# Kernel optimization log

Measured on AMD Instinct MI355X. Metric: run time of the kernel, lower is better.

## Reference

```python
import jax, jax.numpy as jnp
import numpy as np

D_MODEL = 1024
N_HEADS = 16
HEAD_DIM = D_MODEL // N_HEADS
B, S = 2, 2048


def setup_inputs() -> dict:
    key = jax.random.key(0)
    k1, k2, k3, k4, k5 = jax.random.split(key, 5)
    scale = 1.0 / np.sqrt(D_MODEL)
    return {
        "x": jax.random.normal(k1, (B, S, D_MODEL), dtype=jnp.float32),
        "mask": jnp.ones((B, S), dtype=jnp.int32),
        "W_qkv": jax.random.normal(k2, (D_MODEL, 3 * D_MODEL), dtype=jnp.float32) * scale,
        "b_qkv": jnp.zeros((3 * D_MODEL,), dtype=jnp.float32),
        "W_proj": jax.random.normal(k3, (D_MODEL, D_MODEL), dtype=jnp.float32) * scale,
        "b_proj": jnp.zeros((D_MODEL,), dtype=jnp.float32),
    }


def reference(x, mask, W_qkv, b_qkv, W_proj, b_proj):
    b, s, d = x.shape
    qkv = x @ W_qkv + b_qkv                                  # [B,S,3D]
    qkv = qkv.reshape(b, s, 3, N_HEADS, HEAD_DIM)
    qkv = jnp.transpose(qkv, (2, 0, 3, 1, 4))                # [3,B,H,S,Dh]
    q, k, v = qkv[0], qkv[1], qkv[2]
    scores = jnp.einsum("bhqd,bhkd->bhqk", q, k) / np.sqrt(HEAD_DIM)
    if mask is not None:
        m = mask[:, None, None, :]                           # [B,1,1,S]
        scores = jnp.where(m == 0, -jnp.inf, scores)
    attn = jax.nn.softmax(scores, axis=-1)
    out = jnp.einsum("bhqk,bhkd->bhqd", attn, v)             # [B,H,S,Dh]
    out = jnp.transpose(out, (0, 2, 1, 3)).reshape(b, s, d)  # [B,S,D]
    return out @ W_proj + b_proj
```

## Files before the change

kernel.cpp:

```cpp
#include <hip/hip_runtime.h>

typedef unsigned short u16;
typedef unsigned int u32;
typedef __bf16 bf16x8 __attribute__((ext_vector_type(8)));
typedef float f32x4 __attribute__((ext_vector_type(4)));
typedef float f32x16 __attribute__((ext_vector_type(16)));

#define D_MODEL 1024
#define SQ 2048
#define NH 16
#define HD 64
#define QSCALE 0.1803368801111204f

__device__ __forceinline__ u16 f2bf(float f) {
    u32 u = __builtin_bit_cast(u32, f);
    u = (u + 0x7fffu + ((u >> 16) & 1u)) >> 16;
    return (u16)u;
}

__device__ __forceinline__ f32x4 mfma16(bf16x8 a, bf16x8 b, f32x4 c) {
    return __builtin_amdgcn_mfma_f32_16x16x32_bf16(a, b, c, 0, 0, 0);
}
__device__ __forceinline__ f32x16 mfma32(bf16x8 a, bf16x8 b, f32x16 c) {
    return __builtin_amdgcn_mfma_f32_32x32x16_bf16(a, b, c, 0, 0, 0);
}

__device__ __forceinline__ bf16x8 ld16(const void* p) {
    return __builtin_bit_cast(bf16x8, *(const int4*)p);
}

__device__ __forceinline__ void gl_lds16(const u16* g, u16* l) {
    __builtin_amdgcn_global_load_lds((const __attribute__((address_space(1))) unsigned int*)g,
                                     (__attribute__((address_space(3))) unsigned int*)l, 16, 0, 0);
}

__device__ __forceinline__ u32 cvtpk(float a, float b) {
    u32 r;
    asm("v_cvt_pk_bf16_f32 %0, %1, %2" : "=v"(r) : "v"(a), "v"(b));
    return r;
}

__device__ __forceinline__ void swap32(u32& a, u32& b) {
    asm("v_permlane32_swap_b32 %0, %1" : "+v"(a), "+v"(b));
}


__global__ __launch_bounds__(256) void cvt_f32_bf16(const float* __restrict__ in,
                                                    u16* __restrict__ out, int n4) {
    int i = blockIdx.x * blockDim.x + threadIdx.x;
    if (i >= n4) return;
    float4 v = ((const float4*)in)[i];
    ushort4 o;
    o.x = f2bf(v.x); o.y = f2bf(v.y); o.z = f2bf(v.z); o.w = f2bf(v.w);
    ((ushort4*)out)[i] = o;
}

__global__ __launch_bounds__(256) void tconv(const float* __restrict__ in,
                                             u16* __restrict__ out, int K, int N) {
    __shared__ float t[32][33];
    const int n0 = blockIdx.x * 32, k0 = blockIdx.y * 32;
    const int tx = threadIdx.x, ty = threadIdx.y;
#pragma unroll
    for (int i = 0; i < 4; ++i)
        t[ty + 8 * i][tx] = in[(size_t)(k0 + ty + 8 * i) * N + n0 + tx];
    __syncthreads();
#pragma unroll
    for (int i = 0; i < 4; ++i)
        out[(size_t)(n0 + ty + 8 * i) * K + k0 + tx] = f2bf(t[tx][ty + 8 * i]);
}

__global__ __launch_bounds__(256) void vtrans(const u16* __restrict__ Vw, u16* __restrict__ Vtw) {
    __shared__ u16 T[64][72];
    const int bh = blockIdx.y, s0 = blockIdx.x * 64, tid = threadIdx.x;
    const int r = tid >> 3, cb = tid & 7;
#pragma unroll
    for (int i = 0; i < 2; ++i) {
        int rr = r + 32 * i;
        int4 v = *(const int4*)(Vw + ((size_t)bh * SQ + s0 + rr) * HD + cb * 8);
        *(int4*)&T[rr][cb * 8] = v;
    }
    __syncthreads();
#pragma unroll
    for (int i = 0; i < 2; ++i) {
        int d = r + 32 * i, so = cb * 8;
        u16 tmp[8];
#pragma unroll
        for (int j = 0; j < 8; ++j) tmp[j] = T[so + j][d];
        *(int4*)(Vtw + ((size_t)bh * HD + d) * SQ + s0 + so) = *(int4*)tmp;
    }
}


template <int MODE>
__global__ __launch_bounds__(256) void gemm128(const u16* __restrict__ A,
                                               const u16* __restrict__ Bt,
                                               const float* __restrict__ bias,
                                               u16* __restrict__ Qw, u16* __restrict__ Kw,
                                               u16* __restrict__ Vw, float* __restrict__ Out) {
    __shared__ u16 As[128 * 32];
    __shared__ u16 Bs[128 * 32];

    const int tid = threadIdx.x;
    const int l = tid & 63, w = tid >> 6;
    const int l16 = l & 15, lq = l >> 4;
    const int wm = w >> 1, wn = w & 1;
    const int m0 = blockIdx.y * 128, n0 = blockIdx.x * 128;

    f32x4 acc[4][4];
#pragma unroll
    for (int i = 0; i < 4; ++i)
#pragma unroll
        for (int j = 0; j < 4; ++j) acc[i][j] = f32x4{0.f, 0.f, 0.f, 0.f};

    const int srow = 32 * w + (l >> 2);
    const u16* aSrc = A + (size_t)(m0 + srow) * 1024 + (l & 3) * 8;
    const u16* bSrc = Bt + (size_t)(n0 + srow) * 1024 + (l & 3) * 8;
    u16* AsW = As + w * 1024;
    u16* BsW = Bs + w * 1024;

    for (int kt = 0; kt < 32; ++kt) {
        __syncthreads();
        gl_lds16(aSrc + kt * 32, AsW);
        gl_lds16(aSrc + kt * 32 + (size_t)16 * 1024, AsW + 512);
        gl_lds16(bSrc + kt * 32, BsW);
        gl_lds16(bSrc + kt * 32 + (size_t)16 * 1024, BsW + 512);
        __syncthreads();

        bf16x8 af[4], bfr[4];
#pragma unroll
        for (int mi = 0; mi < 4; ++mi)
            af[mi] = ld16((char*)As + (wm * 64 + mi * 16 + l16) * 64 + lq * 16);
#pragma unroll
        for (int ni = 0; ni < 4; ++ni)
            bfr[ni] = ld16((char*)Bs + (wn * 64 + ni * 16 + l16) * 64 + lq * 16);
#pragma unroll
        for (int mi = 0; mi < 4; ++mi)
#pragma unroll
            for (int ni = 0; ni < 4; ++ni)
                acc[mi][ni] = mfma16(af[mi], bfr[ni], acc[mi][ni]);
    }

#pragma unroll
    for (int mi = 0; mi < 4; ++mi) {
#pragma unroll
        for (int ni = 0; ni < 4; ++ni) {
            const int n = n0 + wn * 64 + ni * 16 + l16;
            const float bv = bias[n];
#pragma unroll
            for (int r = 0; r < 4; ++r) {
                const int m = m0 + wm * 64 + mi * 16 + 4 * lq + r;
                float v = acc[mi][ni][r] + bv;
                if (MODE == 0) {
                    const int which = n >> 10;
                    const int h = (n >> 6) & 15;
                    const int d = n & 63;
                    const int b = m >> 11, s = m & 2047;
                    const size_t bh = (size_t)(b * NH + h);
                    if (which == 0)
                        Qw[(bh * SQ + s) * HD + d] = f2bf(v * QSCALE);
                    else if (which == 1)
                        Kw[(bh * SQ + s) * HD + d] = f2bf(v);
                    else
                        Vw[(bh * SQ + s) * HD + d] = f2bf(v);
                } else {
                    Out[(size_t)m * 1024 + n] = v;
                }
            }
        }
    }
}


__global__ __launch_bounds__(256) void gemm_proj(const u16* __restrict__ A,
                                                 const u16* __restrict__ Bt,
                                                 const float* __restrict__ bias,
                                                 float* __restrict__ Out) {
    __shared__ u16 As[128 * 32];
    __shared__ u16 Bs[64 * 32];

    const int tid = threadIdx.x;
    const int l = tid & 63, w = tid >> 6;
    const int l16 = l & 15, lq = l >> 4;
    const int wm = w >> 1, wn = w & 1;
    const int m0 = blockIdx.y * 128, n0 = blockIdx.x * 64;

    f32x4 acc[4][2];
#pragma unroll
    for (int i = 0; i < 4; ++i)
#pragma unroll
        for (int j = 0; j < 2; ++j) acc[i][j] = f32x4{0.f, 0.f, 0.f, 0.f};

    const int srowA = 32 * w + (l >> 2);
    const int srowB = 16 * w + (l >> 2);
    const u16* aSrc = A + (size_t)(m0 + srowA) * 1024 + (l & 3) * 8;
    const u16* bSrc = Bt + (size_t)(n0 + srowB) * 1024 + (l & 3) * 8;
    u16* AsW = As + w * 1024;
    u16* BsW = Bs + w * 512;

    for (int kt = 0; kt < 32; ++kt) {
        __syncthreads();
        gl_lds16(aSrc + kt * 32, AsW);
        gl_lds16(aSrc + kt * 32 + (size_t)16 * 1024, AsW + 512);
        gl_lds16(bSrc + kt * 32, BsW);
        __syncthreads();

        bf16x8 af[4], bfr[2];
#pragma unroll
        for (int mi = 0; mi < 4; ++mi)
            af[mi] = ld16((char*)As + (wm * 64 + mi * 16 + l16) * 64 + lq * 16);
#pragma unroll
        for (int ni = 0; ni < 2; ++ni)
            bfr[ni] = ld16((char*)Bs + (wn * 32 + ni * 16 + l16) * 64 + lq * 16);
#pragma unroll
        for (int mi = 0; mi < 4; ++mi)
#pragma unroll
            for (int ni = 0; ni < 2; ++ni)
                acc[mi][ni] = mfma16(af[mi], bfr[ni], acc[mi][ni]);
    }

#pragma unroll
    for (int mi = 0; mi < 4; ++mi) {
#pragma unroll
        for (int ni = 0; ni < 2; ++ni) {
            const int n = n0 + wn * 32 + ni * 16 + l16;
            const float bv = bias[n];
#pragma unroll
            for (int r = 0; r < 4; ++r) {
                const int m = m0 + wm * 64 + mi * 16 + 4 * lq + r;
                Out[(size_t)m * 1024 + n] = acc[mi][ni][r] + bv;
            }
        }
    }
}


__global__ __launch_bounds__(256, 4) void attn64(const u16* __restrict__ Qw, const u16* __restrict__ Kw,
                                                 const u16* __restrict__ Vtw, const int* __restrict__ mask,
                                                 u16* __restrict__ Ow) {
    __shared__ u16 Ks[2][64 * 64];
    __shared__ u16 Vs[2][64 * 64];
    __shared__ u16 smadd16[SQ];
    __shared__ int allFlag;

    const int tid = threadIdx.x;
    const int l = tid & 63, w = tid >> 6;
    const int q = l & 31, hl = l >> 5;
    const int qh = w & 1, kb = w >> 1;
    const int bh = blockIdx.y, b = bh >> 4, h = bh & 15;
    const int q0 = blockIdx.x * 64;

    if (tid == 0) allFlag = 1;
    __syncthreads();
    {
        const int4* m4 = (const int4*)(mask + (size_t)b * SQ) + tid * 2;
        int4 a0 = m4[0], a1 = m4[1];
        int ok = a0.x && a0.y && a0.z && a0.w && a1.x && a1.y && a1.z && a1.w;
        const u16 NEG = f2bf(-1e30f);
        u16* sp = &smadd16[tid * 8];
        sp[0] = a0.x ? (u16)0 : NEG; sp[1] = a0.y ? (u16)0 : NEG;
        sp[2] = a0.z ? (u16)0 : NEG; sp[3] = a0.w ? (u16)0 : NEG;
        sp[4] = a1.x ? (u16)0 : NEG; sp[5] = a1.y ? (u16)0 : NEG;
        sp[6] = a1.z ? (u16)0 : NEG; sp[7] = a1.w ? (u16)0 : NEG;
        if (!ok) allFlag = 0;
    }

    bf16x8 aq[4];
    {
        const u16* qb = Qw + ((size_t)bh * SQ + q0 + qh * 32 + q) * HD + hl * 8;
#pragma unroll
        for (int kc = 0; kc < 4; ++kc) aq[kc] = ld16(qb + kc * 16);
    }

    const int srow = l >> 3, scb = (l & 7) ^ srow;
    const u16* kbase = Kw + ((size_t)bh * SQ + 16 * w + srow) * HD + scb * 8;
    const u16* vbase = Vtw + ((size_t)bh * HD + 16 * w + srow) * SQ + scb * 8;

    __syncthreads();
    const bool anyMasked = (allFlag == 0);

    {
        u16* kd = (u16*)Ks[0] + w * 1024;
        u16* vd = (u16*)Vs[0] + w * 1024;
#pragma unroll
        for (int j = 0; j < 2; ++j) {
            gl_lds16(kbase + j * 8 * HD, kd + j * 512);
            gl_lds16(vbase + (size_t)j * 8 * SQ, vd + j * 512);
        }
    }
    __syncthreads();

    f32x16 accO[2];
#pragma unroll
    for (int r = 0; r < 16; ++r) { accO[0][r] = 0.f; accO[1][r] = 0.f; }
    float ssum = 0.f;

    const int swzq = (q & 7) << 4;
    const int hb = hl * 16;
    const int krow = 32 * kb + q;

    int p = 0;
    for (int kt = 0; kt < SQ / 64; ++kt) {
        if (kt + 1 < SQ / 64) {
            u16* kd = (u16*)Ks[p ^ 1] + w * 1024;
            u16* vd = (u16*)Vs[p ^ 1] + w * 1024;
            const u16* ks = kbase + (size_t)(kt + 1) * 64 * HD;
            const u16* vs = vbase + (kt + 1) * 64;
#pragma unroll
            for (int j = 0; j < 2; ++j) {
                gl_lds16(ks + j * 8 * HD, kd + j * 512);
                gl_lds16(vs + (size_t)j * 8 * SQ, vd + j * 512);
            }
        }

        const char* Ksp = (const char*)Ks[p];
        const char* Vsp = (const char*)Vs[p];

        f32x16 s;
        if (anyMasked) {
#pragma unroll
            for (int r = 0; r < 16; ++r) {
                int key = kt * 64 + kb * 32 + (r & 3) + 8 * (r >> 2) + 4 * hl;
                u32 bits = (u32)smadd16[key] << 16;
                s[r] = __builtin_bit_cast(float, bits);
            }
        } else {
#pragma unroll
            for (int r = 0; r < 16; ++r) s[r] = 0.f;
        }

        __builtin_amdgcn_s_setprio(1);
#pragma unroll
        for (int kc = 0; kc < 4; ++kc) {
            bf16x8 kf = ld16(Ksp + krow * 128 + ((kc * 32 + hb) ^ swzq));
            s = mfma32(kf, aq[kc], s);
        }
        __builtin_amdgcn_s_setprio(0);

        u32 pw[4][2];
        float r0 = 0.f, r1 = 0.f, r2 = 0.f, r3 = 0.f;
#pragma unroll
        for (int q2 = 0; q2 < 4; ++q2) {
            float p0 = __builtin_amdgcn_exp2f(s[4 * q2 + 0]);
            float p1 = __builtin_amdgcn_exp2f(s[4 * q2 + 1]);
            float p2 = __builtin_amdgcn_exp2f(s[4 * q2 + 2]);
            float p3 = __builtin_amdgcn_exp2f(s[4 * q2 + 3]);
            r0 += p0; r1 += p1; r2 += p2; r3 += p3;
            pw[q2][0] = cvtpk(p0, p1);
            pw[q2][1] = cvtpk(p2, p3);
        }
        float rs = (r0 + r1) + (r2 + r3);
        rs += __shfl_xor(rs, 32);
        ssum += rs;

        bf16x8 pf[2];
#pragma unroll
        for (int c = 0; c < 2; ++c) {
            u32 x0 = pw[2 * c][0], y0 = pw[2 * c + 1][0];
            u32 x1 = pw[2 * c][1], y1 = pw[2 * c + 1][1];
            swap32(x0, y0);
            swap32(x1, y1);
            int4 f;
            f.x = x0; f.y = x1; f.z = y0; f.w = y1;
            pf[c] = __builtin_bit_cast(bf16x8, f);
        }

        __builtin_amdgcn_s_setprio(1);
#pragma unroll
        for (int db = 0; db < 2; ++db) {
            const int vrow = 32 * db + q;
#pragma unroll
            for (int c = 0; c < 2; ++c) {
                bf16x8 vf = ld16(Vsp + vrow * 128 + ((kb * 64 + c * 32 + hb) ^ swzq));
                accO[db] = mfma32(vf, pf[c], accO[db]);
            }
        }
        __builtin_amdgcn_s_setprio(0);

        __syncthreads();
        p ^= 1;
    }

    if (w >= 2) {
        float* ssx = (float*)Vs;
        ssx[qh * 64 + l] = ssum;
        int4* ex = (int4*)Ks + qh * 512 + l;
#pragma unroll
        for (int ch = 0; ch < 8; ++ch) {
            f32x4 qd;
#pragma unroll
            for (int t = 0; t < 4; ++t) qd[t] = accO[ch >> 2][(ch & 3) * 4 + t];
            ex[ch * 64] = __builtin_bit_cast(int4, qd);
        }
    }
    __syncthreads();
    if (w < 2) {
        const float stot = ssum + ((const float*)Vs)[w * 64 + l];
        const float inv = stot > 0.f ? 1.f / stot : 0.f;
        const int4* ex = (const int4*)Ks + w * 512 + l;
#pragma unroll
        for (int ch = 0; ch < 8; ++ch) {
            f32x4 a = __builtin_bit_cast(f32x4, ex[ch * 64]);
#pragma unroll
            for (int t = 0; t < 4; ++t) accO[ch >> 2][(ch & 3) * 4 + t] += a[t];
        }

        u16* ot = (u16*)Vs + 512 + w * 2048;
#pragma unroll
        for (int db = 0; db < 2; ++db)
#pragma unroll
            for (int m = 0; m < 4; ++m) {
                u32 w0 = cvtpk(accO[db][4 * m + 0] * inv, accO[db][4 * m + 1] * inv);
                u32 w1 = cvtpk(accO[db][4 * m + 2] * inv, accO[db][4 * m + 3] * inv);
                const int dbase = 32 * db + 8 * m + 4 * hl;
                uint2 pr; pr.x = w0; pr.y = w1;
                *(uint2*)((char*)ot + q * 128 + ((dbase * 2) ^ ((q & 7) << 4))) = pr;
            }
#pragma unroll
        for (int i = 0; i < 4; ++i) {
            const int qr = 8 * i + (l >> 3);
            int4 vv = *(const int4*)((char*)ot + qr * 128 + (((l & 7) * 16) ^ ((qr & 7) << 4)));
            *(int4*)(Ow + ((size_t)b * SQ + q0 + 32 * w + qr) * D_MODEL + h * HD + (l & 7) * 8) = vv;
        }
    }
}


extern "C" void kernel_launch(void* const* d_in, const int* in_sizes, int n_in,
                              void* d_out, int out_size, void* d_ws, size_t ws_size,
                              hipStream_t stream) {
    (void)in_sizes; (void)n_in; (void)out_size; (void)ws_size;
    const float* x = (const float*)d_in[0];
    const int* mask = (const int*)d_in[1];
    const float* Wqkv = (const float*)d_in[2];
    const float* bqkv = (const float*)d_in[3];
    const float* Wproj = (const float*)d_in[4];
    const float* bproj = (const float*)d_in[5];
    float* out = (float*)d_out;

    char* ws = (char*)d_ws;
    const size_t MB = 1024 * 1024;
    u16* x_bf = (u16*)(ws);
    u16* wq_t = (u16*)(ws + 8 * MB);
    u16* wp_t = (u16*)(ws + 14 * MB);
    u16* Qw   = (u16*)(ws + 16 * MB);
    u16* Kw   = (u16*)(ws + 24 * MB);
    u16* Vtw  = (u16*)(ws + 32 * MB);
    u16* Ow   = (u16*)(ws + 40 * MB);
    u16* Vw   = (u16*)(ws + 40 * MB);

    cvt_f32_bf16<<<4096, 256, 0, stream>>>(x, x_bf, 4096 * 1024 / 4);
    tconv<<<dim3(96, 32), dim3(32, 8), 0, stream>>>(Wqkv, wq_t, 1024, 3072);
    tconv<<<dim3(32, 32), dim3(32, 8), 0, stream>>>(Wproj, wp_t, 1024, 1024);
    gemm128<0><<<dim3(24, 32), 256, 0, stream>>>(x_bf, wq_t, bqkv, Qw, Kw, Vw, nullptr);
    vtrans<<<dim3(32, 32), 256, 0, stream>>>(Vw, Vtw);
    attn64<<<dim3(32, 32), 256, 0, stream>>>(Qw, Kw, Vtw, mask, Ow);
    gemm_proj<<<dim3(16, 32), 256, 0, stream>>>(Ow, wp_t, bproj, out);
}
```

Baseline: 202.6 us.

## Merge prep kernels into one launch and use manual waitcnt barriers in attention

Replaces the separate x conversion and two weight-transpose kernels with a single prep kernel that dispatches work by block index, removing two launches. In the attention loop, __syncthreads is replaced by explicit s_waitcnt vmcnt plus raw s_barrier, so only the previous tile's async LDS loads are waited on while the next tile's loads stay in flight. The per-iteration cross-half row-sum shuffle is also moved out of the loop into a single shuffle at the end. Hand-written waitcnt values carry a correctness risk if the count of outstanding loads does not match what the compiler emits.

```diff
diff --git a/kernel.cpp b/kernel.cpp
--- a/kernel.cpp
+++ b/kernel.cpp
@@ -44,22 +44,40 @@
     asm("v_permlane32_swap_b32 %0, %1" : "+v"(a), "+v"(b));
 }
 
-
-__global__ __launch_bounds__(256) void cvt_f32_bf16(const float* __restrict__ in,
-                                                    u16* __restrict__ out, int n4) {
-    int i = blockIdx.x * blockDim.x + threadIdx.x;
-    if (i >= n4) return;
-    float4 v = ((const float4*)in)[i];
-    ushort4 o;
-    o.x = f2bf(v.x); o.y = f2bf(v.y); o.z = f2bf(v.z); o.w = f2bf(v.w);
-    ((ushort4*)out)[i] = o;
-}
-
-__global__ __launch_bounds__(256) void tconv(const float* __restrict__ in,
-                                             u16* __restrict__ out, int K, int N) {
+__device__ __forceinline__ void barrier_fence() {
+    asm volatile("s_barrier" ::: "memory");
+}
+
+
+__global__ __launch_bounds__(256) void prep(const float* __restrict__ x, u16* __restrict__ x_bf,
+                                            const float* __restrict__ Wqkv, u16* __restrict__ wq_t,
+                                            const float* __restrict__ Wproj, u16* __restrict__ wp_t) {
     __shared__ float t[32][33];
-    const int n0 = blockIdx.x * 32, k0 = blockIdx.y * 32;
-    const int tx = threadIdx.x, ty = threadIdx.y;
+    const int bid = blockIdx.x, tid = threadIdx.x;
+
+    if (bid < 1024) {
+#pragma unroll
+        for (int j = 0; j < 4; ++j) {
+            int i = bid * 1024 + j * 256 + tid;
+            float4 v = ((const float4*)x)[i];
+            ushort4 o;
+            o.x = f2bf(v.x); o.y = f2bf(v.y); o.z = f2bf(v.z); o.w = f2bf(v.w);
+            ((ushort4*)x_bf)[i] = o;
+        }
+        return;
+    }
+
+    const float* in;
+    u16* out;
+    int K = 1024, N, tile;
+    if (bid < 4096) {
+        in = Wqkv; out = wq_t; N = 3072; tile = bid - 1024;
+    } else {
+        in = Wproj; out = wp_t; N = 1024; tile = bid - 4096;
+    }
+    const int nbx = N / 32;
+    const int n0 = (tile % nbx) * 32, k0 = (tile / nbx) * 32;
+    const int tx = tid & 31, ty = tid >> 5;
 #pragma unroll
     for (int i = 0; i < 4; ++i)
         t[ty + 8 * i][tx] = in[(size_t)(k0 + ty + 8 * i) * N + n0 + tx];
@@ -287,7 +305,6 @@
             gl_lds16(vbase + (size_t)j * 8 * SQ, vd + j * 512);
         }
     }
-    __syncthreads();
 
     f32x16 accO[2];
 #pragma unroll
@@ -310,7 +327,11 @@
                 gl_lds16(ks + j * 8 * HD, kd + j * 512);
                 gl_lds16(vs + (size_t)j * 8 * SQ, vd + j * 512);
             }
-        }
+            asm volatile("s_waitcnt vmcnt(4)" ::: "memory");
+        } else {
+            asm volatile("s_waitcnt vmcnt(0)" ::: "memory");
+        }
+        barrier_fence();
 
         const char* Ksp = (const char*)Ks[p];
         const char* Vsp = (const char*)Vs[p];
@@ -348,9 +369,7 @@
             pw[q2][0] = cvtpk(p0, p1);
             pw[q2][1] = cvtpk(p2, p3);
         }
-        float rs = (r0 + r1) + (r2 + r3);
-        rs += __shfl_xor(rs, 32);
-        ssum += rs;
+        ssum += (r0 + r1) + (r2 + r3);
 
         bf16x8 pf[2];
 #pragma unroll
@@ -376,9 +395,11 @@
         }
         __builtin_amdgcn_s_setprio(0);
 
-        __syncthreads();
+        barrier_fence();
         p ^= 1;
     }
+
+    ssum += __shfl_xor(ssum, 32);
 
     if (w >= 2) {
         float* ssx = (float*)Vs;
@@ -448,9 +469,7 @@
     u16* Ow   = (u16*)(ws + 40 * MB);
     u16* Vw   = (u16*)(ws + 40 * MB);
 
-    cvt_f32_bf16<<<4096, 256, 0, stream>>>(x, x_bf, 4096 * 1024 / 4);
-    tconv<<<dim3(96, 32), dim3(32, 8), 0, stream>>>(Wqkv, wq_t, 1024, 3072);
-    tconv<<<dim3(32, 32), dim3(32, 8), 0, stream>>>(Wproj, wp_t, 1024, 1024);
+    prep<<<5120, 256, 0, stream>>>(x, x_bf, Wqkv, wq_t, Wproj, wp_t);
     gemm128<0><<<dim3(24, 32), 256, 0, stream>>>(x_bf, wq_t, bqkv, Qw, Kw, Vw, nullptr);
     vtrans<<<dim3(32, 32), 256, 0, stream>>>(Vw, Vtw);
     attn64<<<dim3(32, 32), 256, 0, stream>>>(Qw, Kw, Vtw, mask, Ow);
```

After: 195.7 us. -3.4%, faster.
